# Kernel optimization log

Hardware: AMD Instinct MI355X
Metric: run time of the kernel (lower is better)

The kernel has to match this reference:

```python
import jax, jax.numpy as jnp
import numpy as np

HIDDEN = 2048
INTER = 5632
NCODES = 4096
VEC = 8
TOKENS = 4096


def dequant(codebook, idx, scale):
    # codebook: [NCODES, VEC]; idx: [out, in//VEC] int32; scale: [out]
    out, ncol = idx.shape
    w = codebook[idx].reshape(out, ncol * VEC)  # [out, in]
    return w * scale[:, None]


def setup_inputs() -> dict:
    key = jax.random.key(0)
    ks = jax.random.split(key, 10)
    return {
        "x": jax.random.normal(ks[0], (TOKENS, HIDDEN), dtype=jnp.float32),
        "codebook_gate": jax.random.normal(ks[1], (NCODES, VEC), dtype=jnp.float32),
        "idx_gate": jax.random.randint(ks[2], (INTER, HIDDEN // VEC), 0, NCODES, dtype=jnp.int32),
        "scale_gate": jax.random.uniform(ks[3], (INTER,), dtype=jnp.float32, minval=0.01, maxval=0.05),
        "codebook_up": jax.random.normal(ks[4], (NCODES, VEC), dtype=jnp.float32),
        "idx_up": jax.random.randint(ks[5], (INTER, HIDDEN // VEC), 0, NCODES, dtype=jnp.int32),
        "scale_up": jax.random.uniform(ks[6], (INTER,), dtype=jnp.float32, minval=0.01, maxval=0.05),
        "codebook_down": jax.random.normal(ks[7], (NCODES, VEC), dtype=jnp.float32),
        "idx_down": jax.random.randint(ks[8], (HIDDEN, INTER // VEC), 0, NCODES, dtype=jnp.int32),
        "scale_down": jax.random.uniform(ks[9], (HIDDEN,), dtype=jnp.float32, minval=0.01, maxval=0.05),
    }


def reference(x, codebook_gate, idx_gate, scale_gate,
              codebook_up, idx_up, scale_up,
              codebook_down, idx_down, scale_down):
    # Dequantize trellis/codebook weights, then SwiGLU:
    # out = down( silu(gate(x)) * up(x) )
    w_gate = dequant(codebook_gate, idx_gate, scale_gate)  # [INTER, HIDDEN]
    w_up = dequant(codebook_up, idx_up, scale_up)          # [INTER, HIDDEN]
    w_down = dequant(codebook_down, idx_down, scale_down)  # [HIDDEN, INTER]
    gate = jax.nn.silu(x @ w_gate.T)                       # [T, INTER]
    up = x @ w_up.T                                        # [T, INTER]
    return (gate * up) @ w_down.T                          # [T, HIDDEN]
```

## Files before the change

### kernel.cpp

```cpp
#include <hip/hip_runtime.h>

#define HIDDEN 2048
#define INTER  5632
#define TOKENS 4096

#define BM 128
#define BN 128
#define BK 64
#define NT2 (INTER / BK)

using bf16x8 = __attribute__((ext_vector_type(8))) __bf16;
using f32x4  = __attribute__((ext_vector_type(4))) float;

__device__ __forceinline__ unsigned short f2bf(float f) {
    unsigned int u = __float_as_uint(f);
    u += 0x7FFFu + ((u >> 16) & 1u);
    return (unsigned short)(u >> 16);
}

#define GLDS(gptr, lptr) \
    __builtin_amdgcn_global_load_lds((__attribute__((address_space(1))) void*)(gptr), \
                                     (__attribute__((address_space(3))) void*)(lptr), 16, 0, 0)

__global__ __launch_bounds__(512) void prep_kernel(
        const float* __restrict__ x, unsigned short* __restrict__ xb,
        const int* __restrict__ ig, const float* __restrict__ cbg,
        const float* __restrict__ sg, unsigned short* __restrict__ wg,
        const int* __restrict__ iu, const float* __restrict__ cbu,
        const float* __restrict__ su, unsigned short* __restrict__ wu,
        const int* __restrict__ idn, const float* __restrict__ cbd,
        const float* __restrict__ sd, unsigned short* __restrict__ wd) {
    __shared__ unsigned short cbl[4096 * 8];
    const int b = blockIdx.x;
    const int tid = threadIdx.x;

    if (b >= 528) {
        int t = (b - 528) * 512 + tid;
        const float4* x4 = (const float4*)x;
        float4 a = x4[2 * t];
        float4 c = x4[2 * t + 1];
        uint4 o;
        o.x = f2bf(a.x) | ((unsigned int)f2bf(a.y) << 16);
        o.y = f2bf(a.z) | ((unsigned int)f2bf(a.w) << 16);
        o.z = f2bf(c.x) | ((unsigned int)f2bf(c.y) << 16);
        o.w = f2bf(c.z) | ((unsigned int)f2bf(c.w) << 16);
        ((uint4*)xb)[t] = o;
        return;
    }

    const int mat = b / 176;
    const int bl  = b % 176;
    const int* idx; const float* cb; const float* scale; unsigned short* w; int ncol8;
    if (mat == 0)      { idx = ig;  cb = cbg; scale = sg; w = wg; ncol8 = HIDDEN / 8; }
    else if (mat == 1) { idx = iu;  cb = cbu; scale = su; w = wu; ncol8 = HIDDEN / 8; }
    else               { idx = idn; cb = cbd; scale = sd; w = wd; ncol8 = INTER / 8; }

    const size_t base = (size_t)bl * 8192;

    int   ids[16];
    float ss[16];
#pragma unroll
    for (int i = 0; i < 16; ++i) {
        size_t t = base + i * 512 + tid;
        ids[i] = idx[t];
        ss[i]  = scale[t / ncol8];
    }

#pragma unroll
    for (int i = 0; i < 8; ++i) {
        int r = i * 512 + tid;
        const float4* c4 = (const float4*)(cb + ((size_t)r << 3));
        float4 a = c4[0];
        float4 c = c4[1];
        uint4 o;
        o.x = f2bf(a.x) | ((unsigned int)f2bf(a.y) << 16);
        o.y = f2bf(a.z) | ((unsigned int)f2bf(a.w) << 16);
        o.z = f2bf(c.x) | ((unsigned int)f2bf(c.y) << 16);
        o.w = f2bf(c.z) | ((unsigned int)f2bf(c.w) << 16);
        ((uint4*)cbl)[r] = o;
    }
    __syncthreads();

#pragma unroll
    for (int i = 0; i < 16; ++i) {
        size_t t = base + i * 512 + tid;
        const unsigned short* cw = cbl + ((unsigned)ids[i] << 3);
        uint4 cv = *(const uint4*)cw;
        float s = ss[i];
        unsigned int ww[4];
#pragma unroll
        for (int j = 0; j < 4; ++j) {
            unsigned int pair = (&cv.x)[j];
            float lo = __uint_as_float(pair << 16) * s;
            float hi = __uint_as_float(pair & 0xFFFF0000u) * s;
            ww[j] = f2bf(lo) | ((unsigned int)f2bf(hi) << 16);
        }
        uint4 o = {ww[0], ww[1], ww[2], ww[3]};
        ((uint4*)w)[t] = o;
    }
}

__device__ __forceinline__ void decode_block(int bid, int nblocks_m, int nblocks_n,
                                             int gN, int* mb, int* nb) {
    int gw = nblocks_m * gN;
    int group = bid / gw;
    int inb = bid % gw;
    int gn = group * gN;
    int width = (nblocks_n - gn < gN) ? (nblocks_n - gn) : gN;
    *mb = inb / width;
    *nb = gn + inb % width;
}

__global__ __launch_bounds__(256, 2) void gemm1_kernel(const unsigned short* __restrict__ X,
                                                       const unsigned short* __restrict__ Wg,
                                                       const unsigned short* __restrict__ Wu,
                                                       unsigned short* __restrict__ H) {
    __shared__ unsigned short As[BM * BK];
    __shared__ unsigned short Bgs[BN * BK];
    __shared__ unsigned short Bus[BN * BK];

    const int tid  = threadIdx.x;
    const int lane = tid & 63;
    const int wave = tid >> 6;
    int mb, nb;
    decode_block(blockIdx.x, TOKENS / BM, INTER / BN, 4, &mb, &nb);
    const int m0 = mb * BM;
    const int n0 = nb * BN;

    const int srow = tid >> 3;
    const int scol = (tid & 7) << 3;
    const int gcol = (((tid & 7) ^ (srow & 7))) << 3;

    const int wr = wave >> 1;
    const int wc = wave & 1;
    const int ln15 = lane & 15;
    const int lq = lane >> 4;
    const int swr = ln15 & 7;

    f32x4 accg[4][4], accu[4][4];
    const f32x4 z = {0.f, 0.f, 0.f, 0.f};
    for (int i = 0; i < 4; ++i)
        for (int j = 0; j < 4; ++j) { accg[i][j] = z; accu[i][j] = z; }

    for (int kt = 0; kt < HIDDEN / BK; ++kt) {
        const int k0 = kt * BK;
        __syncthreads();
#pragma unroll
        for (int i = 0; i < 4; ++i) {
            const int r = i * 32 + srow;
            GLDS(X  + (size_t)(m0 + r) * HIDDEN + k0 + gcol, As  + r * BK + scol);
            GLDS(Wg + (size_t)(n0 + r) * HIDDEN + k0 + gcol, Bgs + r * BK + scol);
            GLDS(Wu + (size_t)(n0 + r) * HIDDEN + k0 + gcol, Bus + r * BK + scol);
        }
        __syncthreads();
#pragma unroll
        for (int ks = 0; ks < 2; ++ks) {
            bf16x8 af[4], bg[4], bu[4];
            const int pofs = (((ks * 4 + lq) ^ swr)) << 3;
#pragma unroll
            for (int im = 0; im < 4; ++im)
                af[im] = *(const bf16x8*)(As + (wr * 64 + im * 16 + ln15) * BK + pofs);
#pragma unroll
            for (int in = 0; in < 4; ++in) {
                bg[in] = *(const bf16x8*)(Bgs + (wc * 64 + in * 16 + ln15) * BK + pofs);
                bu[in] = *(const bf16x8*)(Bus + (wc * 64 + in * 16 + ln15) * BK + pofs);
            }
#pragma unroll
            for (int im = 0; im < 4; ++im)
#pragma unroll
                for (int in = 0; in < 4; ++in) {
                    accg[im][in] = __builtin_amdgcn_mfma_f32_16x16x32_bf16(af[im], bg[in], accg[im][in], 0, 0, 0);
                    accu[im][in] = __builtin_amdgcn_mfma_f32_16x16x32_bf16(af[im], bu[in], accu[im][in], 0, 0, 0);
                }
        }
    }

#pragma unroll
    for (int im = 0; im < 4; ++im)
#pragma unroll
        for (int in = 0; in < 4; ++in) {
            const int row = m0 + wr * 64 + im * 16 + lq * 4;
            const int col = n0 + wc * 64 + in * 16 + ln15;
#pragma unroll
            for (int r = 0; r < 4; ++r) {
                float g = accg[im][in][r];
                float u = accu[im][in][r];
                float h = g * (1.0f / (1.0f + __expf(-g))) * u;
                H[(size_t)(row + r) * INTER + col] = f2bf(h);
            }
        }
}

__global__ __launch_bounds__(256, 2) void gemm2_kernel(const unsigned short* __restrict__ Hin,
                                                       const unsigned short* __restrict__ Wd,
                                                       float* __restrict__ Out) {
    __shared__ unsigned short As[2][BM * BK];
    __shared__ unsigned short Bs[2][BN * BK];

    const int tid  = threadIdx.x;
    const int lane = tid & 63;
    const int wave = tid >> 6;
    int mb, nb;
    decode_block(blockIdx.x, TOKENS / BM, HIDDEN / BN, 2, &mb, &nb);
    const int m0 = mb * BM;
    const int n0 = nb * BN;

    const int srow = tid >> 3;
    const int scol = (tid & 7) << 3;
    const int gcol = (((tid & 7) ^ (srow & 7))) << 3;

    const int wr = wave >> 1;
    const int wc = wave & 1;
    const int ln15 = lane & 15;
    const int lq = lane >> 4;
    const int swr = ln15 & 7;

    f32x4 acc[4][4];
    const f32x4 z = {0.f, 0.f, 0.f, 0.f};
    for (int i = 0; i < 4; ++i)
        for (int j = 0; j < 4; ++j) acc[i][j] = z;

#define STAGE2(buf, kt) do {                                                        \
        const int k0_ = (kt) * BK;                                                  \
        _Pragma("unroll")                                                           \
        for (int i_ = 0; i_ < 4; ++i_) {                                            \
            const int r_ = i_ * 32 + srow;                                          \
            GLDS(Hin + (size_t)(m0 + r_) * INTER + k0_ + gcol,                      \
                 &As[buf][r_ * BK + scol]);                                         \
        }                                                                           \
        _Pragma("unroll")                                                           \
        for (int i_ = 0; i_ < 4; ++i_) {                                            \
            const int r_ = i_ * 32 + srow;                                          \
            GLDS(Wd + (size_t)(n0 + r_) * INTER + k0_ + gcol,                       \
                 &Bs[buf][r_ * BK + scol]);                                         \
        }                                                                           \
    } while (0)

    STAGE2(0, 0);
    STAGE2(1, 1);

    for (int t = 0; t < NT2; ++t) {
        const int cur = t & 1;
        if (t + 1 < NT2) {
            asm volatile("s_waitcnt vmcnt(8)" ::: "memory");
        } else {
            asm volatile("s_waitcnt vmcnt(0)" ::: "memory");
        }
        __builtin_amdgcn_s_barrier();

        bf16x8 a0[4], b0[4];
        {
            const int pofs = ((lq ^ swr)) << 3;
#pragma unroll
            for (int im = 0; im < 4; ++im)
                a0[im] = *(const bf16x8*)(&As[cur][(wr * 64 + im * 16 + ln15) * BK + pofs]);
#pragma unroll
            for (int in = 0; in < 4; ++in)
                b0[in] = *(const bf16x8*)(&Bs[cur][(wc * 64 + in * 16 + ln15) * BK + pofs]);
        }
#pragma unroll
        for (int im = 0; im < 4; ++im)
#pragma unroll
            for (int in = 0; in < 4; ++in)
                acc[im][in] = __builtin_amdgcn_mfma_f32_16x16x32_bf16(a0[im], b0[in], acc[im][in], 0, 0, 0);

        bf16x8 a1[4], b1[4];
        {
            const int pofs = (((4 + lq) ^ swr)) << 3;
#pragma unroll
            for (int im = 0; im < 4; ++im)
                a1[im] = *(const bf16x8*)(&As[cur][(wr * 64 + im * 16 + ln15) * BK + pofs]);
#pragma unroll
            for (int in = 0; in < 4; ++in)
                b1[in] = *(const bf16x8*)(&Bs[cur][(wc * 64 + in * 16 + ln15) * BK + pofs]);
        }
        asm volatile("s_waitcnt lgkmcnt(0)" ::: "memory");
        __builtin_amdgcn_s_barrier();
        if (t + 2 < NT2) STAGE2(cur, t + 2);
#pragma unroll
        for (int im = 0; im < 4; ++im)
#pragma unroll
            for (int in = 0; in < 4; ++in)
                acc[im][in] = __builtin_amdgcn_mfma_f32_16x16x32_bf16(a1[im], b1[in], acc[im][in], 0, 0, 0);
    }
#undef STAGE2

#pragma unroll
    for (int im = 0; im < 4; ++im)
#pragma unroll
        for (int in = 0; in < 4; ++in) {
            const int row = m0 + wr * 64 + im * 16 + lq * 4;
            const int col = n0 + wc * 64 + in * 16 + ln15;
#pragma unroll
            for (int r = 0; r < 4; ++r)
                Out[(size_t)(row + r) * HIDDEN + col] = acc[im][in][r];
        }
}

extern "C" void kernel_launch(void* const* d_in, const int* in_sizes, int n_in,
                              void* d_out, int out_size, void* d_ws, size_t ws_size,
                              hipStream_t stream) {
    (void)in_sizes; (void)n_in; (void)out_size; (void)ws_size;

    const float* x   = (const float*)d_in[0];
    const float* cbg = (const float*)d_in[1];
    const int*   ig  = (const int*)d_in[2];
    const float* sg  = (const float*)d_in[3];
    const float* cbu = (const float*)d_in[4];
    const int*   iu  = (const int*)d_in[5];
    const float* su  = (const float*)d_in[6];
    const float* cbd = (const float*)d_in[7];
    const int*   idn = (const int*)d_in[8];
    const float* sd  = (const float*)d_in[9];
    float* out = (float*)d_out;

    char* p = (char*)d_ws;
    unsigned short* Xb = (unsigned short*)p; p += (size_t)TOKENS * HIDDEN * 2;
    unsigned short* Wg = (unsigned short*)p; p += (size_t)INTER * HIDDEN * 2;
    unsigned short* Wu = (unsigned short*)p; p += (size_t)INTER * HIDDEN * 2;
    unsigned short* Wd = (unsigned short*)p; p += (size_t)HIDDEN * INTER * 2;
    unsigned short* H  = (unsigned short*)p; p += (size_t)TOKENS * INTER * 2;

    prep_kernel<<<dim3(528 + 2048), dim3(512), 0, stream>>>(
        x, Xb, ig, cbg, sg, Wg, iu, cbu, su, Wu, idn, cbd, sd, Wd);

    gemm1_kernel<<<dim3((TOKENS / BM) * (INTER / BN)), dim3(256), 0, stream>>>(Xb, Wg, Wu, H);
    gemm2_kernel<<<dim3((TOKENS / BM) * (HIDDEN / BN)), dim3(256), 0, stream>>>(H, Wd, out);
}
```

Before: 362.0 us.

## Move down-proj dequant into gemm1 grid tail and split x cast kernel

The down-projection weight dequantization now runs in extra blocks appended to the gemm1 grid, so it overlaps the gate/up GEMM instead of lengthening the prep kernel. The x fp32-to-bf16 cast moves into its own kernel, and prep handles only the gate and up weights. The GEMM's shared-memory buffers are unified into one array so the dequant blocks can reuse it for the codebook. The cost is an extra kernel launch and tail blocks in gemm1 that may compete for CUs with GEMM blocks or run last as a serial tail.

```diff
diff --git a/kernel.cpp b/kernel.cpp
--- a/kernel.cpp
+++ b/kernel.cpp
@@ -9,6 +9,9 @@
 #define BK 64
 #define NT2 (INTER / BK)
 
+#define G1B ((TOKENS / BM) * (INTER / BN))
+#define WDB 352
+
 using bf16x8 = __attribute__((ext_vector_type(8))) __bf16;
 using f32x4  = __attribute__((ext_vector_type(4))) float;
 
@@ -22,38 +25,36 @@
     __builtin_amdgcn_global_load_lds((__attribute__((address_space(1))) void*)(gptr), \
                                      (__attribute__((address_space(3))) void*)(lptr), 16, 0, 0)
 
+
+__global__ __launch_bounds__(512) void cast_kernel(const float* __restrict__ x,
+                                                   unsigned short* __restrict__ xb) {
+    int t = blockIdx.x * 512 + threadIdx.x;
+    const float4* x4 = (const float4*)x;
+    float4 a = x4[2 * t];
+    float4 c = x4[2 * t + 1];
+    uint4 o;
+    o.x = f2bf(a.x) | ((unsigned int)f2bf(a.y) << 16);
+    o.y = f2bf(a.z) | ((unsigned int)f2bf(a.w) << 16);
+    o.z = f2bf(c.x) | ((unsigned int)f2bf(c.y) << 16);
+    o.w = f2bf(c.z) | ((unsigned int)f2bf(c.w) << 16);
+    ((uint4*)xb)[t] = o;
+}
+
 __global__ __launch_bounds__(512) void prep_kernel(
-        const float* __restrict__ x, unsigned short* __restrict__ xb,
         const int* __restrict__ ig, const float* __restrict__ cbg,
         const float* __restrict__ sg, unsigned short* __restrict__ wg,
         const int* __restrict__ iu, const float* __restrict__ cbu,
-        const float* __restrict__ su, unsigned short* __restrict__ wu,
-        const int* __restrict__ idn, const float* __restrict__ cbd,
-        const float* __restrict__ sd, unsigned short* __restrict__ wd) {
+        const float* __restrict__ su, unsigned short* __restrict__ wu) {
     __shared__ unsigned short cbl[4096 * 8];
     const int b = blockIdx.x;
     const int tid = threadIdx.x;
 
-    if (b >= 528) {
-        int t = (b - 528) * 512 + tid;
-        const float4* x4 = (const float4*)x;
-        float4 a = x4[2 * t];
-        float4 c = x4[2 * t + 1];
-        uint4 o;
-        o.x = f2bf(a.x) | ((unsigned int)f2bf(a.y) << 16);
-        o.y = f2bf(a.z) | ((unsigned int)f2bf(a.w) << 16);
-        o.z = f2bf(c.x) | ((unsigned int)f2bf(c.y) << 16);
-        o.w = f2bf(c.z) | ((unsigned int)f2bf(c.w) << 16);
-        ((uint4*)xb)[t] = o;
-        return;
-    }
-
     const int mat = b / 176;
     const int bl  = b % 176;
-    const int* idx; const float* cb; const float* scale; unsigned short* w; int ncol8;
-    if (mat == 0)      { idx = ig;  cb = cbg; scale = sg; w = wg; ncol8 = HIDDEN / 8; }
-    else if (mat == 1) { idx = iu;  cb = cbu; scale = su; w = wu; ncol8 = HIDDEN / 8; }
-    else               { idx = idn; cb = cbd; scale = sd; w = wd; ncol8 = INTER / 8; }
+    const int* idx; const float* cb; const float* scale; unsigned short* w;
+    if (mat == 0) { idx = ig; cb = cbg; scale = sg; w = wg; }
+    else          { idx = iu; cb = cbu; scale = su; w = wu; }
+    const int ncol8 = HIDDEN / 8;
 
     const size_t base = (size_t)bl * 8192;
 
@@ -114,12 +115,66 @@
 __global__ __launch_bounds__(256, 2) void gemm1_kernel(const unsigned short* __restrict__ X,
                                                        const unsigned short* __restrict__ Wg,
                                                        const unsigned short* __restrict__ Wu,
-                                                       unsigned short* __restrict__ H) {
-    __shared__ unsigned short As[BM * BK];
-    __shared__ unsigned short Bgs[BN * BK];
-    __shared__ unsigned short Bus[BN * BK];
+                                                       unsigned short* __restrict__ H,
+                                                       const int* __restrict__ idn,
+                                                       const float* __restrict__ cbd,
+                                                       const float* __restrict__ sd,
+                                                       unsigned short* __restrict__ Wd) {
+    __shared__ unsigned short smem[32768];
 
     const int tid  = threadIdx.x;
+
+    if (blockIdx.x >= G1B) {
+        const int bl = blockIdx.x - G1B;
+        const size_t base = (size_t)bl * 4096;
+        const int ncol8 = INTER / 8;
+
+        int   ids[16];
+        float ss[16];
+#pragma unroll
+        for (int i = 0; i < 16; ++i) {
+            size_t t = base + i * 256 + tid;
+            ids[i] = idn[t];
+            ss[i]  = sd[t / ncol8];
+        }
+#pragma unroll
+        for (int i = 0; i < 16; ++i) {
+            int r = i * 256 + tid;
+            const float4* c4 = (const float4*)(cbd + ((size_t)r << 3));
+            float4 a = c4[0];
+            float4 c = c4[1];
+            uint4 o;
+            o.x = f2bf(a.x) | ((unsigned int)f2bf(a.y) << 16);
+            o.y = f2bf(a.z) | ((unsigned int)f2bf(a.w) << 16);
+            o.z = f2bf(c.x) | ((unsigned int)f2bf(c.y) << 16);
+            o.w = f2bf(c.z) | ((unsigned int)f2bf(c.w) << 16);
+            ((uint4*)smem)[r] = o;
+        }
+        __syncthreads();
+#pragma unroll
+        for (int i = 0; i < 16; ++i) {
+            size_t t = base + i * 256 + tid;
+            const unsigned short* cw = smem + ((unsigned)ids[i] << 3);
+            uint4 cv = *(const uint4*)cw;
+            float s = ss[i];
+            unsigned int ww[4];
+#pragma unroll
+            for (int j = 0; j < 4; ++j) {
+                unsigned int pair = (&cv.x)[j];
+                float lo = __uint_as_float(pair << 16) * s;
+                float hi = __uint_as_float(pair & 0xFFFF0000u) * s;
+                ww[j] = f2bf(lo) | ((unsigned int)f2bf(hi) << 16);
+            }
+            uint4 o = {ww[0], ww[1], ww[2], ww[3]};
+            ((uint4*)Wd)[t] = o;
+        }
+        return;
+    }
+
+    unsigned short* As  = smem;
+    unsigned short* Bgs = smem + 8192;
+    unsigned short* Bus = smem + 16384;
+
     const int lane = tid & 63;
     const int wave = tid >> 6;
     int mb, nb;
@@ -321,9 +376,10 @@
     unsigned short* Wd = (unsigned short*)p; p += (size_t)HIDDEN * INTER * 2;
     unsigned short* H  = (unsigned short*)p; p += (size_t)TOKENS * INTER * 2;
 
-    prep_kernel<<<dim3(528 + 2048), dim3(512), 0, stream>>>(
-        x, Xb, ig, cbg, sg, Wg, iu, cbu, su, Wu, idn, cbd, sd, Wd);
-
-    gemm1_kernel<<<dim3((TOKENS / BM) * (INTER / BN)), dim3(256), 0, stream>>>(Xb, Wg, Wu, H);
+    cast_kernel<<<dim3(TOKENS * HIDDEN / 8 / 512), dim3(512), 0, stream>>>(x, Xb);
+    prep_kernel<<<dim3(352), dim3(512), 0, stream>>>(ig, cbg, sg, Wg, iu, cbu, su, Wu);
+
+    gemm1_kernel<<<dim3(G1B + WDB), dim3(256), 0, stream>>>(Xb, Wg, Wu, H,
+                                                            idn, cbd, sd, Wd);
     gemm2_kernel<<<dim3((TOKENS / BM) * (HIDDEN / BN)), dim3(256), 0, stream>>>(H, Wd, out);
 }
```

Result: slower. 375.0 us (+3.6%).
